# Performance work log

Hardware: AMD Instinct MI355X
Metric: run time of the kernel (lower is better)

## Reference

```python
import jax, jax.numpy as jnp
import numpy as np

D_MODEL = 1024
N_HEADS = 16
D_K = D_MODEL // N_HEADS
NEG_INF = -1.0e9


def setup_inputs() -> dict:
    key = jax.random.key(0)
    ks = jax.random.split(key, 12)
    B, S = 2, 2048
    inp = {
        "q": jax.random.normal(ks[0], (B, S, D_MODEL), dtype=jnp.float32),
        "k": jax.random.normal(ks[1], (B, S, D_MODEL), dtype=jnp.float32),
        "v": jax.random.normal(ks[2], (B, S, D_MODEL), dtype=jnp.float32),
        "mask": jax.random.randint(ks[3], (B, 1, S, S), 0, 2, dtype=jnp.int32),
        "Wq": jax.random.normal(ks[4], (D_MODEL, D_MODEL), dtype=jnp.float32) / np.sqrt(D_MODEL),
        "bq": jnp.zeros((D_MODEL,), dtype=jnp.float32),
        "Wk": jax.random.normal(ks[5], (D_MODEL, D_MODEL), dtype=jnp.float32) / np.sqrt(D_MODEL),
        "bk": jnp.zeros((D_MODEL,), dtype=jnp.float32),
        "Wv": jax.random.normal(ks[6], (D_MODEL, D_MODEL), dtype=jnp.float32) / np.sqrt(D_MODEL),
        "bv": jnp.zeros((D_MODEL,), dtype=jnp.float32),
        "Wo": jax.random.normal(ks[7], (D_MODEL, D_MODEL), dtype=jnp.float32) / np.sqrt(D_MODEL),
        "bo": jnp.zeros((D_MODEL,), dtype=jnp.float32),
    }
    return inp


def _split_heads(x):
    B, S, _ = x.shape
    return x.reshape(B, S, N_HEADS, D_K).transpose(0, 2, 1, 3)  # [B,H,S,Dk]


def reference(q, k, v, mask, Wq, bq, Wk, bk, Wv, bv, Wo, bo):
    # QKV projections (nn.Linear: x @ W.T + b; here W stored as [in,out]-agnostic square)
    query = _split_heads(q @ Wq + bq)
    key_ = _split_heads(k @ Wk + bk)
    value = _split_heads(v @ Wv + bv)

    scale = 1.0 / np.sqrt(D_K).astype(np.float32)
    scores = jnp.einsum("bhqd,bhkd->bhqk", query, key_) * scale  # [B,H,S,S]
    scores = jnp.where(mask == 0, NEG_INF, scores)
    attn = jax.nn.softmax(scores, axis=-1)  # dropout is identity in eval (p=0.0)
    ctx = jnp.einsum("bhqk,bhkd->bhqd", attn, value)  # [B,H,S,Dk]

    B, H, S, Dk = ctx.shape
    ctx = ctx.transpose(0, 2, 1, 3).reshape(B, S, H * Dk)
    return ctx @ Wo + bo
```

## Files before the change

kernel.cpp:

```cpp
#include <hip/hip_runtime.h>
#include <hip/hip_bf16.h>

typedef __bf16 bf16_t;
typedef __bf16 bf16x2 __attribute__((ext_vector_type(2)));
typedef __bf16 bf16x8 __attribute__((ext_vector_type(8)));
typedef float f32x4 __attribute__((ext_vector_type(4)));
typedef float f32x16 __attribute__((ext_vector_type(16)));
typedef unsigned int u32;
typedef unsigned long long u64;

#define S_LEN 2048
#define DM 1024
#define NH 16
#define DK 64
#define M_ROWS 4096
#define SCALE_LOG2E 0.1803368801111204f

__device__ __forceinline__ int sw_off(int row, int col) {
  return row * 64 + ((((col >> 3) ^ row) & 7) << 3) + (col & 7);
}

__device__ __forceinline__ bf16x8 cvt8(const float4& a, const float4& b) {
  bf16x8 v;
  v[0] = (__bf16)a.x; v[1] = (__bf16)a.y; v[2] = (__bf16)a.z; v[3] = (__bf16)a.w;
  v[4] = (__bf16)b.x; v[5] = (__bf16)b.y; v[6] = (__bf16)b.z; v[7] = (__bf16)b.w;
  return v;
}

__device__ __forceinline__ void glds16(const bf16_t* g, bf16_t* l) {
  __builtin_amdgcn_global_load_lds(
      (const __attribute__((address_space(1))) void*)g,
      (__attribute__((address_space(3))) void*)l, 16, 0, 0);
}

__global__ __launch_bounds__(256) void pack_maskT(
    const int* __restrict__ mask, u64* __restrict__ mbT)
{
  const int g = blockIdx.x * 256 + threadIdx.x;
  const int key = g & 2047;
  const int qw = (g >> 11) & 31;
  const int b = g >> 16;
  const int* src = &mask[((size_t)b * S_LEN + qw * 64) * S_LEN + key];
  u64 bits = 0;
  #pragma unroll
  for (int i = 0; i < 64; ++i)
    bits |= (u64)(src[(size_t)i * S_LEN] != 0) << i;
  mbT[g] = bits;
}

__global__ __launch_bounds__(256) void cvt_inputs(
    const float* __restrict__ q, const float* __restrict__ k,
    const float* __restrict__ v, bf16_t* __restrict__ Xb)
{
  const int z = blockIdx.y;
  const float* __restrict__ src = (z == 0) ? q : ((z == 1) ? k : v);
  const size_t idx = ((size_t)blockIdx.x * 256 + threadIdx.x) * 8;
  const float4 a = *(const float4*)&src[idx];
  const float4 b = *(const float4*)&src[idx + 4];
  *(bf16x8*)&Xb[(size_t)z * M_ROWS * DM + idx] = cvt8(a, b);
}

__global__ __launch_bounds__(256) void transw_kernel(
    const float* __restrict__ Wq, const float* __restrict__ Wk,
    const float* __restrict__ Wv, const float* __restrict__ Wo,
    bf16_t* __restrict__ Wt)
{
  const int z = blockIdx.z;
  const float* __restrict__ W = (z == 0) ? Wq : ((z == 1) ? Wk : ((z == 2) ? Wv : Wo));
  bf16_t* __restrict__ out = Wt + (size_t)z * DM * DM;
  __shared__ float tile[64][65];
  const int tx = threadIdx.x & 31, ty = threadIdx.x >> 5;
  const int k0 = blockIdx.x * 64, n0 = blockIdx.y * 64;
  #pragma unroll
  for (int j = 0; j < 8; ++j) {
    const float2 v = *(const float2*)&W[(size_t)(k0 + ty + 8 * j) * DM + n0 + tx * 2];
    tile[ty + 8 * j][tx * 2] = v.x;
    tile[ty + 8 * j][tx * 2 + 1] = v.y;
  }
  __syncthreads();
  #pragma unroll
  for (int j = 0; j < 8; ++j) {
    const int a = ty + 8 * j;
    bf16x2 p;
    p[0] = (__bf16)tile[tx * 2][a];
    p[1] = (__bf16)tile[tx * 2 + 1][a];
    *(bf16x2*)&out[(size_t)(n0 + a) * DM + k0 + tx * 2] = p;
  }
}

__device__ __forceinline__ void gemm128_body(
    const bf16_t* __restrict__ A, const bf16_t* __restrict__ Bt,
    const float* __restrict__ bias, bf16_t* __restrict__ outb,
    float* __restrict__ outf)
{
  __shared__ __align__(16) bf16_t As[128 * 32];
  __shared__ __align__(16) bf16_t Bs[128 * 32];
  const int t = threadIdx.x, w = t >> 6, L = t & 63, quad = L >> 4, l16 = L & 15;
  const int m0 = blockIdx.x * 128, n0 = blockIdx.y * 128;
  const int mb = 64 * (w & 1), nb = 64 * (w >> 1);
  const int rowS = t >> 2, subS = (t & 3) * 8;

  f32x4 acc[4][4] = {};
  for (int k0 = 0; k0 < DM; k0 += 32) {
    __syncthreads();
    glds16(&A[(size_t)(m0 + rowS) * DM + k0 + subS],        &As[t * 8]);
    glds16(&A[(size_t)(m0 + 64 + rowS) * DM + k0 + subS],   &As[2048 + t * 8]);
    glds16(&Bt[(size_t)(n0 + rowS) * DM + k0 + subS],       &Bs[t * 8]);
    glds16(&Bt[(size_t)(n0 + 64 + rowS) * DM + k0 + subS],  &Bs[2048 + t * 8]);
    __syncthreads();
    bf16x8 af[4], bfr[4];
    #pragma unroll
    for (int mt = 0; mt < 4; ++mt)
      af[mt] = *(const bf16x8*)&As[(mb + 16 * mt + l16) * 32 + quad * 8];
    #pragma unroll
    for (int ct = 0; ct < 4; ++ct)
      bfr[ct] = *(const bf16x8*)&Bs[(nb + 16 * ct + l16) * 32 + quad * 8];
    #pragma unroll
    for (int mt = 0; mt < 4; ++mt)
      #pragma unroll
      for (int ct = 0; ct < 4; ++ct)
        acc[mt][ct] = __builtin_amdgcn_mfma_f32_16x16x32_bf16(af[mt], bfr[ct], acc[mt][ct], 0, 0, 0);
  }
  #pragma unroll
  for (int mt = 0; mt < 4; ++mt)
    #pragma unroll
    for (int ct = 0; ct < 4; ++ct)
      #pragma unroll
      for (int r = 0; r < 4; ++r) {
        const int row = m0 + mb + 16 * mt + quad * 4 + r;
        const int n = n0 + nb + 16 * ct + l16;
        const float val = acc[mt][ct][r] + bias[n];
        if (outb) outb[(size_t)row * DM + n] = (__bf16)val;
        else      outf[(size_t)row * DM + n] = val;
      }
}

__global__ __launch_bounds__(256) void gemm_qkv(
    const bf16_t* __restrict__ Xb, const bf16_t* __restrict__ Wt,
    const float* __restrict__ bq, const float* __restrict__ bk,
    const float* __restrict__ bv, bf16_t* __restrict__ QKVb)
{
  const int z = blockIdx.z;
  gemm128_body(Xb + (size_t)z * M_ROWS * DM, Wt + (size_t)z * DM * DM,
               (z == 0) ? bq : ((z == 1) ? bk : bv),
               QKVb + (size_t)z * M_ROWS * DM, nullptr);
}

__global__ __launch_bounds__(256) void gemm_out(
    const bf16_t* __restrict__ ctx, const bf16_t* __restrict__ Wto,
    const float* __restrict__ bo, float* __restrict__ out)
{
  gemm128_body(ctx, Wto, bo, nullptr, out);
}

__global__ __launch_bounds__(256) void transpV(
    const bf16_t* __restrict__ Vb, bf16_t* __restrict__ Vtw)
{
  __shared__ bf16_t Tr[64 * 72];
  const int t = threadIdx.x;
  const int key0 = blockIdx.x * 64;
  const int bh = blockIdx.y, b = bh >> 4, h = bh & 15;
  const int r = t >> 2, c = (t & 3) * 16;
  const bf16_t* src = &Vb[(size_t)(b * S_LEN + key0 + r) * DM + h * DK + c];
  const bf16x8 v0 = *(const bf16x8*)src;
  const bf16x8 v1 = *(const bf16x8*)(src + 8);
  #pragma unroll
  for (int j = 0; j < 8; ++j) {
    Tr[r * 72 + c + j] = v0[j];
    Tr[r * 72 + c + 8 + j] = v1[j];
  }
  __syncthreads();
  const int dv = t >> 2, kc = (t & 3) * 16;
  bf16_t ov[16];
  #pragma unroll
  for (int j = 0; j < 16; ++j) ov[j] = Tr[(kc + j) * 72 + dv];
  bf16_t* dst = &Vtw[((size_t)bh * DK + dv) * S_LEN + key0 + kc];
  *(bf16x8*)dst = *(bf16x8*)&ov[0];
  *(bf16x8*)(dst + 8) = *(bf16x8*)&ov[8];
}

__global__ __launch_bounds__(256, 2) void attn_kernel(
    const bf16_t* __restrict__ Qb, const bf16_t* __restrict__ Kb,
    const bf16_t* __restrict__ Vtw, const u64* __restrict__ mbT,
    bf16_t* __restrict__ ctx)
{
  __shared__ __align__(16) bf16_t Qs[128 * 64];
  __shared__ __align__(16) bf16_t Ks[64 * 64];
  __shared__ __align__(16) bf16_t Vts[64 * 64];
  __shared__ __align__(16) bf16_t Ps[128 * 64];

  const int t = threadIdx.x, w = t >> 6, L = t & 63;
  const int l31 = L & 31, h5 = L >> 5;
  const int q0 = blockIdx.x * 128;
  const int bh = blockIdx.y, b = bh >> 4, h = bh & 15;
  const int sr = t >> 2, sc = (t & 3) * 16;

  #pragma unroll
  for (int half = 0; half < 2; ++half) {
    const int row = half * 64 + sr;
    const bf16_t* s = &Qb[(size_t)(b * S_LEN + q0 + row) * DM + h * DK + sc];
    *(bf16x8*)&Qs[sw_off(row, sc)]     = *(const bf16x8*)s;
    *(bf16x8*)&Qs[sw_off(row, sc + 8)] = *(const bf16x8*)(s + 8);
  }

  const int qw = 2 * blockIdx.x + (w >> 1);
  const size_t mrow = ((size_t)b * 32 + qw) * 2048;

  bf16x8 kp0, kp1, vp0, vp1;
  u64 mp[2];
  {
    const bf16_t* sk = &Kb[(size_t)(b * S_LEN + sr) * DM + h * DK + sc];
    kp0 = *(const bf16x8*)sk; kp1 = *(const bf16x8*)(sk + 8);
    const bf16_t* sv = &Vtw[((size_t)bh * DK + sr) * S_LEN + sc];
    vp0 = *(const bf16x8*)sv; vp1 = *(const bf16x8*)(sv + 8);
    #pragma unroll
    for (int nt = 0; nt < 2; ++nt) mp[nt] = mbT[mrow + nt * 32 + l31];
  }

  f32x16 O[2] = {};
  float l_part[16];
  #pragma unroll
  for (int r = 0; r < 16; ++r) l_part[r] = 0.f;

  const int shbase = 4 * h5;

  for (int kt = 0; kt < S_LEN / 64; ++kt) {
    __syncthreads();
    *(bf16x8*)&Ks[sw_off(sr, sc)]      = kp0;
    *(bf16x8*)&Ks[sw_off(sr, sc + 8)]  = kp1;
    *(bf16x8*)&Vts[sw_off(sr, sc)]     = vp0;
    *(bf16x8*)&Vts[sw_off(sr, sc + 8)] = vp1;
    u64 mcur0 = mp[0], mcur1 = mp[1];
    __syncthreads();

    if (kt + 1 < S_LEN / 64) {
      const int key1 = (kt + 1) * 64;
      const bf16_t* sk = &Kb[(size_t)(b * S_LEN + key1 + sr) * DM + h * DK + sc];
      kp0 = *(const bf16x8*)sk; kp1 = *(const bf16x8*)(sk + 8);
      const bf16_t* sv = &Vtw[((size_t)bh * DK + sr) * S_LEN + key1 + sc];
      vp0 = *(const bf16x8*)sv; vp1 = *(const bf16x8*)(sv + 8);
      #pragma unroll
      for (int nt = 0; nt < 2; ++nt) mp[nt] = mbT[mrow + key1 + nt * 32 + l31];
    }

    f32x16 sacc[2] = {};
    #pragma unroll
    for (int ks = 0; ks < 4; ++ks) {
      const bf16x8 a = *(const bf16x8*)&Qs[sw_off(32 * w + l31, ks * 16 + 8 * h5)];
      #pragma unroll
      for (int nt = 0; nt < 2; ++nt) {
        const bf16x8 bb = *(const bf16x8*)&Ks[sw_off(nt * 32 + l31, ks * 16 + 8 * h5)];
        sacc[nt] = __builtin_amdgcn_mfma_f32_32x32x16_bf16(a, bb, sacc[nt], 0, 0, 0);
      }
    }

    const u32 m32_0 = (u32)((w & 1) ? (mcur0 >> 32) : mcur0) >> shbase;
    const u32 m32_1 = (u32)((w & 1) ? (mcur1 >> 32) : mcur1) >> shbase;
    #pragma unroll
    for (int r = 0; r < 16; ++r) {
      const int c = (r & 3) + 8 * (r >> 2);
      const int prow = 32 * w + c + 4 * h5;
      float p0 = __builtin_exp2f(__builtin_fmaf(sacc[0][r], SCALE_LOG2E, -16.f));
      float p1 = __builtin_exp2f(__builtin_fmaf(sacc[1][r], SCALE_LOG2E, -16.f));
      p0 = ((m32_0 >> c) & 1u) ? p0 : 0.f;
      p1 = ((m32_1 >> c) & 1u) ? p1 : 0.f;
      l_part[r] += p0 + p1;
      Ps[sw_off(prow, l31)]      = (__bf16)p0;
      Ps[sw_off(prow, 32 + l31)] = (__bf16)p1;
    }

    #pragma unroll
    for (int kk = 0; kk < 4; ++kk) {
      const bf16x8 a = *(const bf16x8*)&Ps[sw_off(32 * w + l31, kk * 16 + 8 * h5)];
      #pragma unroll
      for (int nt = 0; nt < 2; ++nt) {
        const bf16x8 bb = *(const bf16x8*)&Vts[sw_off(nt * 32 + l31, kk * 16 + 8 * h5)];
        O[nt] = __builtin_amdgcn_mfma_f32_32x32x16_bf16(a, bb, O[nt], 0, 0, 0);
      }
    }
  }

  #pragma unroll
  for (int r = 0; r < 16; ++r) {
    float s = l_part[r];
    s += __shfl_xor(s, 1);
    s += __shfl_xor(s, 2);
    s += __shfl_xor(s, 4);
    s += __shfl_xor(s, 8);
    s += __shfl_xor(s, 16);
    const float inv = 1.f / s;
    const int rowg = q0 + 32 * w + (r & 3) + 8 * (r >> 2) + 4 * h5;
    #pragma unroll
    for (int nt = 0; nt < 2; ++nt) {
      const int col = h * DK + nt * 32 + l31;
      ctx[(size_t)(b * S_LEN + rowg) * DM + col] = (__bf16)(O[nt][r] * inv);
    }
  }
}

extern "C" void kernel_launch(void* const* d_in, const int* in_sizes, int n_in,
                              void* d_out, int out_size, void* d_ws, size_t ws_size,
                              hipStream_t stream) {
  const float* q  = (const float*)d_in[0];
  const float* k  = (const float*)d_in[1];
  const float* v  = (const float*)d_in[2];
  const int* mask = (const int*)d_in[3];
  const float* Wq = (const float*)d_in[4];
  const float* bq = (const float*)d_in[5];
  const float* Wk = (const float*)d_in[6];
  const float* bk = (const float*)d_in[7];
  const float* Wv = (const float*)d_in[8];
  const float* bv = (const float*)d_in[9];
  const float* Wo = (const float*)d_in[10];
  const float* bo = (const float*)d_in[11];
  float* out = (float*)d_out;

  const size_t SLICE = (size_t)M_ROWS * DM;
  bf16_t* Xb   = (bf16_t*)d_ws;
  bf16_t* QKVb = Xb + 3 * SLICE;
  bf16_t* Wt   = QKVb + 3 * SLICE;
  u64* mbT     = (u64*)(Wt + (size_t)4 * DM * DM);
  bf16_t* ctx  = Xb;
  bf16_t* Vtw  = Xb + SLICE;

  pack_maskT<<<dim3(512), dim3(256), 0, stream>>>(mask, mbT);
  cvt_inputs<<<dim3(2048, 3), dim3(256), 0, stream>>>(q, k, v, Xb);
  transw_kernel<<<dim3(16, 16, 4), dim3(256), 0, stream>>>(Wq, Wk, Wv, Wo, Wt);
  gemm_qkv<<<dim3(32, 8, 3), dim3(256), 0, stream>>>(Xb, Wt, bq, bk, bv, QKVb);
  transpV<<<dim3(32, 32), dim3(256), 0, stream>>>(QKVb + 2 * SLICE, Vtw);
  attn_kernel<<<dim3(16, 32), dim3(256), 0, stream>>>(QKVb, QKVb + SLICE, Vtw, mbT, ctx);
  gemm_out<<<dim3(32, 8), dim3(256), 0, stream>>>(ctx, Wt + (size_t)3 * DM * DM, bo, out);
}
```

Baseline: 290.9 us.

## Split attention over key halves with pre-swizzled K/V tiles and merge kernel

Splits the attention key loop into two halves across grid z, writing unnormalized partial outputs and row sums that a new merge kernel combines and normalizes. K and V^T are written in pre-swizzled 64x64 tiles so the attention kernel can load them with global_load_lds directly. The softmax scale is folded into the Q projection epilogue, row sums are computed with an extra MFMA against a ones vector, and the mask is applied with bitwise ANDs. The mask pack kernel now reads int4 vectors. This adds occupancy and parallelism at the cost of an extra partial-output round trip through memory and one more launch, and it removes the register prefetch of the next K/V tile.

```diff
diff --git a/kernel.cpp b/kernel.cpp
--- a/kernel.cpp
+++ b/kernel.cpp
@@ -33,19 +33,44 @@
       (__attribute__((address_space(3))) void*)l, 16, 0, 0);
 }
 
+__device__ __forceinline__ u32 bitmask32(u32 m, int c) {
+  return (u32)(((int)(m << (31 - c))) >> 31);
+}
+__device__ __forceinline__ float mand(float p, u32 e) {
+  return __builtin_bit_cast(float, __builtin_bit_cast(u32, p) & e);
+}
+__device__ __forceinline__ u32 pack2(float lo, float hi) {
+#if __has_builtin(__builtin_amdgcn_cvt_pk_bf16_f32)
+  bf16x2 r = __builtin_amdgcn_cvt_pk_bf16_f32(lo, hi);
+  return __builtin_bit_cast(u32, r);
+#else
+  union { __bf16 h[2]; u32 u; } x;
+  x.h[0] = (__bf16)lo; x.h[1] = (__bf16)hi;
+  return x.u;
+#endif
+}
+
+union U4B { uint4 u; bf16x8 v; };
+
 __global__ __launch_bounds__(256) void pack_maskT(
     const int* __restrict__ mask, u64* __restrict__ mbT)
 {
   const int g = blockIdx.x * 256 + threadIdx.x;
-  const int key = g & 2047;
-  const int qw = (g >> 11) & 31;
-  const int b = g >> 16;
-  const int* src = &mask[((size_t)b * S_LEN + qw * 64) * S_LEN + key];
-  u64 bits = 0;
-  #pragma unroll
-  for (int i = 0; i < 64; ++i)
-    bits |= (u64)(src[(size_t)i * S_LEN] != 0) << i;
-  mbT[g] = bits;
+  const int key4 = (g & 511) * 4;
+  const int qw = (g >> 9) & 31;
+  const int b = g >> 14;
+  const int* src = &mask[((size_t)b * S_LEN + qw * 64) * S_LEN + key4];
+  u64 b0 = 0, b1 = 0, b2 = 0, b3 = 0;
+  #pragma unroll 8
+  for (int i = 0; i < 64; ++i) {
+    const int4 v = *(const int4*)&src[(size_t)i * S_LEN];
+    b0 |= (u64)(v.x != 0) << i;
+    b1 |= (u64)(v.y != 0) << i;
+    b2 |= (u64)(v.z != 0) << i;
+    b3 |= (u64)(v.w != 0) << i;
+  }
+  u64* dst = &mbT[((size_t)b * 32 + qw) * S_LEN + key4];
+  dst[0] = b0; dst[1] = b1; dst[2] = b2; dst[3] = b3;
 }
 
 __global__ __launch_bounds__(256) void cvt_inputs(
@@ -88,10 +113,9 @@
   }
 }
 
-__device__ __forceinline__ void gemm128_body(
+__device__ __forceinline__ void gemm_core(
     const bf16_t* __restrict__ A, const bf16_t* __restrict__ Bt,
-    const float* __restrict__ bias, bf16_t* __restrict__ outb,
-    float* __restrict__ outf)
+    f32x4 (&acc)[4][4])
 {
   __shared__ __align__(16) bf16_t As[128 * 32];
   __shared__ __align__(16) bf16_t Bs[128 * 32];
@@ -100,13 +124,12 @@
   const int mb = 64 * (w & 1), nb = 64 * (w >> 1);
   const int rowS = t >> 2, subS = (t & 3) * 8;
 
-  f32x4 acc[4][4] = {};
   for (int k0 = 0; k0 < DM; k0 += 32) {
     __syncthreads();
-    glds16(&A[(size_t)(m0 + rowS) * DM + k0 + subS],        &As[t * 8]);
-    glds16(&A[(size_t)(m0 + 64 + rowS) * DM + k0 + subS],   &As[2048 + t * 8]);
-    glds16(&Bt[(size_t)(n0 + rowS) * DM + k0 + subS],       &Bs[t * 8]);
-    glds16(&Bt[(size_t)(n0 + 64 + rowS) * DM + k0 + subS],  &Bs[2048 + t * 8]);
+    glds16(&A[(size_t)(m0 + rowS) * DM + k0 + subS],       &As[t * 8]);
+    glds16(&A[(size_t)(m0 + 64 + rowS) * DM + k0 + subS],  &As[2048 + t * 8]);
+    glds16(&Bt[(size_t)(n0 + rowS) * DM + k0 + subS],      &Bs[t * 8]);
+    glds16(&Bt[(size_t)(n0 + 64 + rowS) * DM + k0 + subS], &Bs[2048 + t * 8]);
     __syncthreads();
     bf16x8 af[4], bfr[4];
     #pragma unroll
@@ -121,6 +144,22 @@
       for (int ct = 0; ct < 4; ++ct)
         acc[mt][ct] = __builtin_amdgcn_mfma_f32_16x16x32_bf16(af[mt], bfr[ct], acc[mt][ct], 0, 0, 0);
   }
+}
+
+__global__ __launch_bounds__(256) void gemm_qkv(
+    const bf16_t* __restrict__ Xb, const bf16_t* __restrict__ Wt,
+    const float* __restrict__ bq, const float* __restrict__ bk,
+    const float* __restrict__ bv,
+    bf16_t* __restrict__ Qp, bf16_t* __restrict__ Ksw, bf16_t* __restrict__ Vpl)
+{
+  const int z = blockIdx.z;
+  const float* __restrict__ bias = (z == 0) ? bq : ((z == 1) ? bk : bv);
+  f32x4 acc[4][4] = {};
+  gemm_core(Xb + (size_t)z * M_ROWS * DM, Wt + (size_t)z * DM * DM, acc);
+
+  const int t = threadIdx.x, w = t >> 6, L = t & 63, quad = L >> 4, l16 = L & 15;
+  const int m0 = blockIdx.x * 128, n0 = blockIdx.y * 128;
+  const int mb = 64 * (w & 1), nb = 64 * (w >> 1);
   #pragma unroll
   for (int mt = 0; mt < 4; ++mt)
     #pragma unroll
@@ -129,39 +168,28 @@
       for (int r = 0; r < 4; ++r) {
         const int row = m0 + mb + 16 * mt + quad * 4 + r;
         const int n = n0 + nb + 16 * ct + l16;
-        const float val = acc[mt][ct][r] + bias[n];
-        if (outb) outb[(size_t)row * DM + n] = (__bf16)val;
-        else      outf[(size_t)row * DM + n] = val;
+        float val = acc[mt][ct][r] + bias[n];
+        if (z == 0) {
+          Qp[(size_t)row * DM + n] = (__bf16)(val * SCALE_LOG2E);
+        } else if (z == 2) {
+          Vpl[(size_t)row * DM + n] = (__bf16)val;
+        } else {
+          const int b_ = row >> 11, s = row & 2047, h = n >> 6, d = n & 63;
+          const int bh = b_ * NH + h;
+          Ksw[((size_t)bh * 32 + (s >> 6)) * 4096 + sw_off(s & 63, d)] = (__bf16)val;
+        }
       }
 }
 
-__global__ __launch_bounds__(256) void gemm_qkv(
-    const bf16_t* __restrict__ Xb, const bf16_t* __restrict__ Wt,
-    const float* __restrict__ bq, const float* __restrict__ bk,
-    const float* __restrict__ bv, bf16_t* __restrict__ QKVb)
-{
-  const int z = blockIdx.z;
-  gemm128_body(Xb + (size_t)z * M_ROWS * DM, Wt + (size_t)z * DM * DM,
-               (z == 0) ? bq : ((z == 1) ? bk : bv),
-               QKVb + (size_t)z * M_ROWS * DM, nullptr);
-}
-
-__global__ __launch_bounds__(256) void gemm_out(
-    const bf16_t* __restrict__ ctx, const bf16_t* __restrict__ Wto,
-    const float* __restrict__ bo, float* __restrict__ out)
-{
-  gemm128_body(ctx, Wto, bo, nullptr, out);
-}
-
 __global__ __launch_bounds__(256) void transpV(
-    const bf16_t* __restrict__ Vb, bf16_t* __restrict__ Vtw)
+    const bf16_t* __restrict__ Vpl, bf16_t* __restrict__ Vt_sw)
 {
   __shared__ bf16_t Tr[64 * 72];
   const int t = threadIdx.x;
   const int key0 = blockIdx.x * 64;
   const int bh = blockIdx.y, b = bh >> 4, h = bh & 15;
   const int r = t >> 2, c = (t & 3) * 16;
-  const bf16_t* src = &Vb[(size_t)(b * S_LEN + key0 + r) * DM + h * DK + c];
+  const bf16_t* src = &Vpl[(size_t)(b * S_LEN + key0 + r) * DM + h * DK + c];
   const bf16x8 v0 = *(const bf16x8*)src;
   const bf16x8 v1 = *(const bf16x8*)(src + 8);
   #pragma unroll
@@ -174,128 +202,150 @@
   bf16_t ov[16];
   #pragma unroll
   for (int j = 0; j < 16; ++j) ov[j] = Tr[(kc + j) * 72 + dv];
-  bf16_t* dst = &Vtw[((size_t)bh * DK + dv) * S_LEN + key0 + kc];
-  *(bf16x8*)dst = *(bf16x8*)&ov[0];
-  *(bf16x8*)(dst + 8) = *(bf16x8*)&ov[8];
-}
-
-__global__ __launch_bounds__(256, 2) void attn_kernel(
-    const bf16_t* __restrict__ Qb, const bf16_t* __restrict__ Kb,
-    const bf16_t* __restrict__ Vtw, const u64* __restrict__ mbT,
-    bf16_t* __restrict__ ctx)
-{
-  __shared__ __align__(16) bf16_t Qs[128 * 64];
-  __shared__ __align__(16) bf16_t Ks[64 * 64];
-  __shared__ __align__(16) bf16_t Vts[64 * 64];
-  __shared__ __align__(16) bf16_t Ps[128 * 64];
+  bf16_t* dst = &Vt_sw[((size_t)bh * 32 + blockIdx.x) * 4096];
+  *(bf16x8*)&dst[sw_off(dv, kc)]     = *(bf16x8*)&ov[0];
+  *(bf16x8*)&dst[sw_off(dv, kc + 8)] = *(bf16x8*)&ov[8];
+}
+
+__global__ __launch_bounds__(256, 4) void attn_kernel(
+    const bf16_t* __restrict__ Qp, const bf16_t* __restrict__ Ksw,
+    const bf16_t* __restrict__ Vt_sw, const u64* __restrict__ mbT,
+    bf16_t* __restrict__ Of, float* __restrict__ Lf)
+{
+  __shared__ __align__(16) bf16_t Ks[4096];
+  __shared__ __align__(16) bf16_t Vts[4096];
+  __shared__ __align__(16) u32 Psd[4096];
 
   const int t = threadIdx.x, w = t >> 6, L = t & 63;
   const int l31 = L & 31, h5 = L >> 5;
   const int q0 = blockIdx.x * 128;
   const int bh = blockIdx.y, b = bh >> 4, h = bh & 15;
-  const int sr = t >> 2, sc = (t & 3) * 16;
-
-  #pragma unroll
-  for (int half = 0; half < 2; ++half) {
-    const int row = half * 64 + sr;
-    const bf16_t* s = &Qb[(size_t)(b * S_LEN + q0 + row) * DM + h * DK + sc];
-    *(bf16x8*)&Qs[sw_off(row, sc)]     = *(const bf16x8*)s;
-    *(bf16x8*)&Qs[sw_off(row, sc + 8)] = *(const bf16x8*)(s + 8);
-  }
-
-  const int qw = 2 * blockIdx.x + (w >> 1);
-  const size_t mrow = ((size_t)b * 32 + qw) * 2048;
-
-  bf16x8 kp0, kp1, vp0, vp1;
-  u64 mp[2];
+  const int split = blockIdx.z;
+  const int xk3 = (l31 & 7) << 3;
+  const u32 sel = (l31 & 1) ? 0x07060302u : 0x05040100u;
+
+  bf16x8 qf[4];
   {
-    const bf16_t* sk = &Kb[(size_t)(b * S_LEN + sr) * DM + h * DK + sc];
-    kp0 = *(const bf16x8*)sk; kp1 = *(const bf16x8*)(sk + 8);
-    const bf16_t* sv = &Vtw[((size_t)bh * DK + sr) * S_LEN + sc];
-    vp0 = *(const bf16x8*)sv; vp1 = *(const bf16x8*)(sv + 8);
-    #pragma unroll
-    for (int nt = 0; nt < 2; ++nt) mp[nt] = mbT[mrow + nt * 32 + l31];
-  }
-
-  f32x16 O[2] = {};
-  float l_part[16];
-  #pragma unroll
-  for (int r = 0; r < 16; ++r) l_part[r] = 0.f;
-
-  const int shbase = 4 * h5;
-
-  for (int kt = 0; kt < S_LEN / 64; ++kt) {
+    const bf16_t* qrow = &Qp[((size_t)(b * S_LEN) + q0 + 32 * w + l31) * DM + h * DK + 8 * h5];
+    #pragma unroll
+    for (int ks = 0; ks < 4; ++ks) qf[ks] = *(const bf16x8*)&qrow[16 * ks];
+  }
+
+  bf16x8 ones;
+  #pragma unroll
+  for (int j = 0; j < 8; ++j) ones[j] = (__bf16)1.0f;
+
+  const int qw = (q0 >> 6) + (w >> 1);
+  const size_t mrow = ((size_t)b * 32 + qw) * S_LEN;
+  const int bitc = 32 * (w & 1) + 4 * h5;
+
+  const bf16_t* Kbase = Ksw + (size_t)bh * 32 * 4096;
+  const bf16_t* Vbase = Vt_sw + (size_t)bh * 32 * 4096;
+
+  f32x16 O0 = {}, O1 = {}, Lacc = {};
+
+  for (int kt = split * 16; kt < split * 16 + 16; ++kt) {
     __syncthreads();
-    *(bf16x8*)&Ks[sw_off(sr, sc)]      = kp0;
-    *(bf16x8*)&Ks[sw_off(sr, sc + 8)]  = kp1;
-    *(bf16x8*)&Vts[sw_off(sr, sc)]     = vp0;
-    *(bf16x8*)&Vts[sw_off(sr, sc + 8)] = vp1;
-    u64 mcur0 = mp[0], mcur1 = mp[1];
+    glds16(Kbase + (size_t)kt * 4096 + t * 8,        &Ks[t * 8]);
+    glds16(Kbase + (size_t)kt * 4096 + 2048 + t * 8, &Ks[2048 + t * 8]);
+    glds16(Vbase + (size_t)kt * 4096 + t * 8,        &Vts[t * 8]);
+    glds16(Vbase + (size_t)kt * 4096 + 2048 + t * 8, &Vts[2048 + t * 8]);
+    const u64 mq0 = mbT[mrow + kt * 64 + l31];
+    const u64 mq1 = mbT[mrow + kt * 64 + 32 + l31];
     __syncthreads();
 
-    if (kt + 1 < S_LEN / 64) {
-      const int key1 = (kt + 1) * 64;
-      const bf16_t* sk = &Kb[(size_t)(b * S_LEN + key1 + sr) * DM + h * DK + sc];
-      kp0 = *(const bf16x8*)sk; kp1 = *(const bf16x8*)(sk + 8);
-      const bf16_t* sv = &Vtw[((size_t)bh * DK + sr) * S_LEN + key1 + sc];
-      vp0 = *(const bf16x8*)sv; vp1 = *(const bf16x8*)(sv + 8);
+    f32x16 s0 = {}, s1 = {};
+    #pragma unroll
+    for (int ks = 0; ks < 4; ++ks) {
+      const int ko = ((2 * ks + h5) << 3) ^ xk3;
+      const bf16x8 kb0 = *(const bf16x8*)&Ks[l31 * 64 + ko];
+      const bf16x8 kb1 = *(const bf16x8*)&Ks[(32 + l31) * 64 + ko];
+      s0 = __builtin_amdgcn_mfma_f32_32x32x16_bf16(qf[ks], kb0, s0, 0, 0, 0);
+      s1 = __builtin_amdgcn_mfma_f32_32x32x16_bf16(qf[ks], kb1, s1, 0, 0, 0);
+    }
+
+    const u32 m32_0 = (u32)(mq0 >> bitc);
+    const u32 m32_1 = (u32)(mq1 >> bitc);
+    #pragma unroll
+    for (int rp = 0; rp < 16; rp += 2) {
+      const int c = (rp & 3) + 8 * (rp >> 2);
+      const int qp = 16 * w + (c >> 1) + 2 * h5;
+      float p00 = mand(__builtin_exp2f(s0[rp]),     bitmask32(m32_0, c));
+      float p01 = mand(__builtin_exp2f(s0[rp + 1]), bitmask32(m32_0, c + 1));
+      float p10 = mand(__builtin_exp2f(s1[rp]),     bitmask32(m32_1, c));
+      float p11 = mand(__builtin_exp2f(s1[rp + 1]), bitmask32(m32_1, c + 1));
+      Psd[qp * 64 + ((((l31 >> 3) ^ qp) & 7) << 3) + (l31 & 7)]         = pack2(p00, p01);
+      Psd[qp * 64 + (((((l31 >> 3) + 4) ^ qp) & 7) << 3) + (l31 & 7)]   = pack2(p10, p11);
+    }
+
+    const int qpr = 16 * w + (l31 >> 1);
+    #pragma unroll
+    for (int kk = 0; kk < 4; ++kk) {
+      const int ch = ((2 * kk + h5) ^ qpr) & 7;
+      const uint4 lo = *(const uint4*)&Psd[qpr * 64 + ch * 8];
+      const uint4 hi = *(const uint4*)&Psd[qpr * 64 + ch * 8 + 4];
+      U4B af;
+      af.u.x = __builtin_amdgcn_perm(lo.y, lo.x, sel);
+      af.u.y = __builtin_amdgcn_perm(lo.w, lo.z, sel);
+      af.u.z = __builtin_amdgcn_perm(hi.y, hi.x, sel);
+      af.u.w = __builtin_amdgcn_perm(hi.w, hi.z, sel);
+      const int vo = ((2 * kk + h5) << 3) ^ xk3;
+      const bf16x8 vb0 = *(const bf16x8*)&Vts[l31 * 64 + vo];
+      const bf16x8 vb1 = *(const bf16x8*)&Vts[(32 + l31) * 64 + vo];
+      O0 = __builtin_amdgcn_mfma_f32_32x32x16_bf16(af.v, vb0, O0, 0, 0, 0);
+      O1 = __builtin_amdgcn_mfma_f32_32x32x16_bf16(af.v, vb1, O1, 0, 0, 0);
+      Lacc = __builtin_amdgcn_mfma_f32_32x32x16_bf16(af.v, ones, Lacc, 0, 0, 0);
+    }
+  }
+
+  #pragma unroll
+  for (int r = 0; r < 16; ++r) {
+    const int row = q0 + 32 * w + (r & 3) + 8 * (r >> 2) + 4 * h5;
+    const size_t obase = (((size_t)split * M_ROWS) + b * S_LEN + row) * DM + h * DK;
+    Of[obase + l31]      = (__bf16)O0[r];
+    Of[obase + 32 + l31] = (__bf16)O1[r];
+    if (l31 == 0)
+      Lf[((size_t)split * M_ROWS + b * S_LEN + row) * NH + h] = Lacc[r];
+  }
+}
+
+__global__ __launch_bounds__(256) void merge_kernel(
+    const bf16_t* __restrict__ Of, const float* __restrict__ Lf,
+    bf16_t* __restrict__ ctx)
+{
+  const size_t idx = ((size_t)blockIdx.x * 256 + threadIdx.x) * 8;
+  const int row = (int)(idx >> 10);
+  const int h = (int)((idx >> 6) & 15);
+  const float l = Lf[(size_t)row * NH + h] + Lf[(size_t)M_ROWS * NH + (size_t)row * NH + h];
+  const float inv = 1.0f / l;
+  const bf16x8 o0 = *(const bf16x8*)&Of[idx];
+  const bf16x8 o1 = *(const bf16x8*)&Of[(size_t)M_ROWS * DM + idx];
+  bf16x8 r;
+  #pragma unroll
+  for (int j = 0; j < 8; ++j)
+    r[j] = (__bf16)(((float)o0[j] + (float)o1[j]) * inv);
+  *(bf16x8*)&ctx[idx] = r;
+}
+
+__global__ __launch_bounds__(256) void gemm_out(
+    const bf16_t* __restrict__ ctx, const bf16_t* __restrict__ Wto,
+    const float* __restrict__ bo, float* __restrict__ out)
+{
+  f32x4 acc[4][4] = {};
+  gemm_core(ctx, Wto, acc);
+  const int t = threadIdx.x, w = t >> 6, L = t & 63, quad = L >> 4, l16 = L & 15;
+  const int m0 = blockIdx.x * 128, n0 = blockIdx.y * 128;
+  const int mb = 64 * (w & 1), nb = 64 * (w >> 1);
+  #pragma unroll
+  for (int mt = 0; mt < 4; ++mt)
+    #pragma unroll
+    for (int ct = 0; ct < 4; ++ct)
       #pragma unroll
-      for (int nt = 0; nt < 2; ++nt) mp[nt] = mbT[mrow + key1 + nt * 32 + l31];
-    }
-
-    f32x16 sacc[2] = {};
-    #pragma unroll
-    for (int ks = 0; ks < 4; ++ks) {
-      const bf16x8 a = *(const bf16x8*)&Qs[sw_off(32 * w + l31, ks * 16 + 8 * h5)];
-      #pragma unroll
-      for (int nt = 0; nt < 2; ++nt) {
-        const bf16x8 bb = *(const bf16x8*)&Ks[sw_off(nt * 32 + l31, ks * 16 + 8 * h5)];
-        sacc[nt] = __builtin_amdgcn_mfma_f32_32x32x16_bf16(a, bb, sacc[nt], 0, 0, 0);
+      for (int r = 0; r < 4; ++r) {
+        const int row = m0 + mb + 16 * mt + quad * 4 + r;
+        const int n = n0 + nb + 16 * ct + l16;
+        out[(size_t)row * DM + n] = acc[mt][ct][r] + bo[n];
       }
-    }
-
-    const u32 m32_0 = (u32)((w & 1) ? (mcur0 >> 32) : mcur0) >> shbase;
-    const u32 m32_1 = (u32)((w & 1) ? (mcur1 >> 32) : mcur1) >> shbase;
-    #pragma unroll
-    for (int r = 0; r < 16; ++r) {
-      const int c = (r & 3) + 8 * (r >> 2);
-      const int prow = 32 * w + c + 4 * h5;
-      float p0 = __builtin_exp2f(__builtin_fmaf(sacc[0][r], SCALE_LOG2E, -16.f));
-      float p1 = __builtin_exp2f(__builtin_fmaf(sacc[1][r], SCALE_LOG2E, -16.f));
-      p0 = ((m32_0 >> c) & 1u) ? p0 : 0.f;
-      p1 = ((m32_1 >> c) & 1u) ? p1 : 0.f;
-      l_part[r] += p0 + p1;
-      Ps[sw_off(prow, l31)]      = (__bf16)p0;
-      Ps[sw_off(prow, 32 + l31)] = (__bf16)p1;
-    }
-
-    #pragma unroll
-    for (int kk = 0; kk < 4; ++kk) {
-      const bf16x8 a = *(const bf16x8*)&Ps[sw_off(32 * w + l31, kk * 16 + 8 * h5)];
-      #pragma unroll
-      for (int nt = 0; nt < 2; ++nt) {
-        const bf16x8 bb = *(const bf16x8*)&Vts[sw_off(nt * 32 + l31, kk * 16 + 8 * h5)];
-        O[nt] = __builtin_amdgcn_mfma_f32_32x32x16_bf16(a, bb, O[nt], 0, 0, 0);
-      }
-    }
-  }
-
-  #pragma unroll
-  for (int r = 0; r < 16; ++r) {
-    float s = l_part[r];
-    s += __shfl_xor(s, 1);
-    s += __shfl_xor(s, 2);
-    s += __shfl_xor(s, 4);
-    s += __shfl_xor(s, 8);
-    s += __shfl_xor(s, 16);
-    const float inv = 1.f / s;
-    const int rowg = q0 + 32 * w + (r & 3) + 8 * (r >> 2) + 4 * h5;
-    #pragma unroll
-    for (int nt = 0; nt < 2; ++nt) {
-      const int col = h * DK + nt * 32 + l31;
-      ctx[(size_t)(b * S_LEN + rowg) * DM + col] = (__bf16)(O[nt][r] * inv);
-    }
-  }
 }
 
 extern "C" void kernel_launch(void* const* d_in, const int* in_sizes, int n_in,
@@ -316,18 +366,24 @@
   float* out = (float*)d_out;
 
   const size_t SLICE = (size_t)M_ROWS * DM;
-  bf16_t* Xb   = (bf16_t*)d_ws;
-  bf16_t* QKVb = Xb + 3 * SLICE;
-  bf16_t* Wt   = QKVb + 3 * SLICE;
-  u64* mbT     = (u64*)(Wt + (size_t)4 * DM * DM);
-  bf16_t* ctx  = Xb;
-  bf16_t* Vtw  = Xb + SLICE;
-
-  pack_maskT<<<dim3(512), dim3(256), 0, stream>>>(mask, mbT);
+  bf16_t* ws_b = (bf16_t*)d_ws;
+  bf16_t* Xb    = ws_b;
+  bf16_t* Qp    = ws_b + 3 * SLICE;
+  bf16_t* Ksw   = ws_b + 4 * SLICE;
+  bf16_t* Vpl   = ws_b + 5 * SLICE;
+  bf16_t* Wt    = ws_b + 6 * SLICE;
+  u64* mbT      = (u64*)(ws_b + 7 * SLICE);
+  float* Lf     = (float*)((char*)mbT + (1 << 20));
+  bf16_t* Of    = ws_b;
+  bf16_t* Vt_sw = ws_b + 2 * SLICE;
+  bf16_t* ctx   = ws_b + 2 * SLICE;
+
+  pack_maskT<<<dim3(128), dim3(256), 0, stream>>>(mask, mbT);
   cvt_inputs<<<dim3(2048, 3), dim3(256), 0, stream>>>(q, k, v, Xb);
   transw_kernel<<<dim3(16, 16, 4), dim3(256), 0, stream>>>(Wq, Wk, Wv, Wo, Wt);
-  gemm_qkv<<<dim3(32, 8, 3), dim3(256), 0, stream>>>(Xb, Wt, bq, bk, bv, QKVb);
-  transpV<<<dim3(32, 32), dim3(256), 0, stream>>>(QKVb + 2 * SLICE, Vtw);
-  attn_kernel<<<dim3(16, 32), dim3(256), 0, stream>>>(QKVb, QKVb + SLICE, Vtw, mbT, ctx);
+  gemm_qkv<<<dim3(32, 8, 3), dim3(256), 0, stream>>>(Xb, Wt, bq, bk, bv, Qp, Ksw, Vpl);
+  transpV<<<dim3(32, 32), dim3(256), 0, stream>>>(Vpl, Vt_sw);
+  attn_kernel<<<dim3(16, 32, 2), dim3(256), 0, stream>>>(Qp, Ksw, Vt_sw, mbT, Of, Lf);
+  merge_kernel<<<dim3(2048), dim3(256), 0, stream>>>(Of, Lf, ctx);
   gemm_out<<<dim3(32, 8), dim3(256), 0, stream>>>(ctx, Wt + (size_t)3 * DM * DM, bo, out);
 }
```

Result: slower. 349.4 us (+20.1%).
